# Performance work log

Measured on AMD Instinct MI355X. Metric: run time of the kernel, lower is better.

## Reference

```python
import jax, jax.numpy as jnp
import numpy as np

B, S = 128, 524288  # batch, seq_len; S % target_len == 0 so rounded boundaries are uniform


def setup_inputs() -> dict:
    key = jax.random.key(0)
    x = jax.random.normal(key, (B, S), dtype=jnp.float32)
    return {"x": x, "target_len": 256}


def reference(x, target_len):
    # Original loops over target_len segments with boundaries
    # start=round(i*S/target_len), end=round((i+1)*S/target_len).
    # With S % target_len == 0 these are exactly uniform with L = S // target_len
    # (>1), so each segment's change strength is mean(|diff|) over L-1 gaps.
    b, s = x.shape
    L = s // target_len  # segment length (2048 here)
    seg = x.reshape(b, target_len, L)            # [B, T, L]
    d = jnp.abs(jnp.diff(seg, axis=2))           # [B, T, L-1]
    return d.mean(axis=2)                        # [B, T]
```

## Files before the change

### kernel.cpp

```cpp
#include <hip/hip_runtime.h>

#define SEG_LEN 2048
#define GAPS_INV (1.0f / 2047.0f)

__global__ __launch_bounds__(256)
void seg_change_strength_kernel(const float* __restrict__ x,
                                float* __restrict__ out) {
    const int t = threadIdx.x;
    const long long segBase = (long long)blockIdx.x * SEG_LEN;
    const float* p = x + segBase + (long long)t * 8;

    const float4 v0 = *(const float4*)(p);
    const float4 v1 = *(const float4*)(p + 4);
    const float nxt = (t < 255) ? p[8] : v1.w;

    float s = fabsf(v0.y - v0.x) + fabsf(v0.z - v0.y) + fabsf(v0.w - v0.z)
            + fabsf(v1.x - v0.w) + fabsf(v1.y - v1.x) + fabsf(v1.z - v1.y)
            + fabsf(v1.w - v1.z) + fabsf(nxt  - v1.w);

    #pragma unroll
    for (int off = 32; off > 0; off >>= 1)
        s += __shfl_down(s, off, 64);

    __shared__ float wsum[4];
    if ((t & 63) == 0) wsum[t >> 6] = s;
    __syncthreads();
    if (t == 0)
        out[blockIdx.x] = (wsum[0] + wsum[1] + wsum[2] + wsum[3]) * GAPS_INV;
}

extern "C" void kernel_launch(void* const* d_in, const int* in_sizes, int n_in,
                              void* d_out, int out_size, void* d_ws, size_t ws_size,
                              hipStream_t stream) {
    const float* x = (const float*)d_in[0];
    float* out = (float*)d_out;
    const int n = in_sizes[0];
    const int nseg = n / SEG_LEN;
    seg_change_strength_kernel<<<nseg, 256, 0, stream>>>(x, out);
}
```

Baseline: 345.1 us.

## Assign one wavefront per segment with grid-stride loop and coalesced float4 loads

```diff
diff --git a/kernel.cpp b/kernel.cpp
--- a/kernel.cpp
+++ b/kernel.cpp
@@ -5,28 +5,42 @@
 
 __global__ __launch_bounds__(256)
 void seg_change_strength_kernel(const float* __restrict__ x,
-                                float* __restrict__ out) {
-    const int t = threadIdx.x;
-    const long long segBase = (long long)blockIdx.x * SEG_LEN;
-    const float* p = x + segBase + (long long)t * 8;
+                                float* __restrict__ out, int nseg) {
+    const int lane   = threadIdx.x & 63;
+    const int nwaves = (gridDim.x * 256) >> 6;
+    const int wid    = blockIdx.x * 4 + (threadIdx.x >> 6);
 
-    const float4 v0 = *(const float4*)(p);
-    const float4 v1 = *(const float4*)(p + 4);
-    const float nxt = (t < 255) ? p[8] : v1.w;
+    for (int seg = wid; seg < nseg; seg += nwaves) {
+        const float4* p = (const float4*)(x + (long long)seg * SEG_LEN);
 
-    float s = fabsf(v0.y - v0.x) + fabsf(v0.z - v0.y) + fabsf(v0.w - v0.z)
-            + fabsf(v1.x - v0.w) + fabsf(v1.y - v1.x) + fabsf(v1.z - v1.y)
-            + fabsf(v1.w - v1.z) + fabsf(nxt  - v1.w);
+        float4 f[8];
+        #pragma unroll
+        for (int c = 0; c < 8; ++c)
+            f[c] = p[c * 64 + lane];
 
-    #pragma unroll
-    for (int off = 32; off > 0; off >>= 1)
-        s += __shfl_down(s, off, 64);
+        float s = 0.0f;
+        #pragma unroll
+        for (int c = 0; c < 8; ++c) {
+            s += fabsf(f[c].y - f[c].x)
+               + fabsf(f[c].z - f[c].y)
+               + fabsf(f[c].w - f[c].z);
+            float nx = __shfl_down(f[c].x, 1, 64);
+            float nxt;
+            if (c < 7) {
+                float wrap = __shfl(f[c + 1].x, 0, 64);
+                nxt = (lane == 63) ? wrap : nx;
+            } else {
+                nxt = (lane == 63) ? f[7].w : nx;
+            }
+            s += fabsf(nxt - f[c].w);
+        }
 
-    __shared__ float wsum[4];
-    if ((t & 63) == 0) wsum[t >> 6] = s;
-    __syncthreads();
-    if (t == 0)
-        out[blockIdx.x] = (wsum[0] + wsum[1] + wsum[2] + wsum[3]) * GAPS_INV;
+        #pragma unroll
+        for (int off = 32; off > 0; off >>= 1)
+            s += __shfl_down(s, off, 64);
+
+        if (lane == 0) out[seg] = s * GAPS_INV;
+    }
 }
 
 extern "C" void kernel_launch(void* const* d_in, const int* in_sizes, int n_in,
@@ -36,5 +50,8 @@
     float* out = (float*)d_out;
     const int n = in_sizes[0];
     const int nseg = n / SEG_LEN;
-    seg_change_strength_kernel<<<nseg, 256, 0, stream>>>(x, out);
+
+    int blocks = (nseg + 3) / 4;
+    if (blocks > 4096) blocks = 4096;
+    seg_change_strength_kernel<<<blocks, 256, 0, stream>>>(x, out, nseg);
 }
```

After: 352.5 us. 1.02x slower.
